# Kernel optimization log

Measured on AMD Instinct MI355X. Metric: run time of the kernel, lower is better.

## Reference

```python
import jax, jax.numpy as jnp
import numpy as np

H = 1024   # hidden_size
A = 16     # number_ab (branches)
O = 4      # num_outputs per branch
B = 4096   # batch
P = 2048   # number of selected rows
EPS = 1e-5


def setup_inputs() -> dict:
    key = jax.random.key(0)
    ks = jax.random.split(key, 12)
    s = 0.02  # weight init scale
    inp = {
        "X": jax.random.normal(ks[0], (B, H), jnp.float32),
        "X1": jax.random.normal(ks[1], (B, H), jnp.float32),
        # stacked per-branch parameters (batched over antibody axis A)
        "W1": jax.random.normal(ks[2], (A, H, H), jnp.float32) * s,
        "b1": jnp.zeros((A, H), jnp.float32),
        "W2": jax.random.normal(ks[3], (A, H, H), jnp.float32) * s,
        "b2": jnp.zeros((A, H), jnp.float32),
        "W3": jax.random.normal(ks[4], (A, H, H), jnp.float32) * s,
        "b3": jnp.zeros((A, H), jnp.float32),
        "gamma": jnp.ones((A, H), jnp.float32),
        "beta": jnp.zeros((A, H), jnp.float32),
        "W4": jax.random.normal(ks[5], (A, H, O), jnp.float32) * s,
        "b4": jnp.zeros((A, O), jnp.float32),
        "positions_y": jax.random.randint(ks[6], (P,), 0, B, jnp.int32),
    }
    return inp


def reference(X, X1, W1, b1, W2, b2, W3, b3, gamma, beta, W4, b4, positions_y):
    # z = l1(X) + l2(X1) per branch, batched over A: [B, A, H]
    z = (jnp.einsum('bh,aho->bao', X, W1) + b1
         + jnp.einsum('bh,aho->bao', X1, W2) + b2)
    # mlm: Linear -> ReLU -> LayerNorm -> Linear
    h = jax.nn.relu(jnp.einsum('bah,aho->bao', z, W3) + b3)  # [B, A, H]
    mu = jnp.mean(h, axis=-1, keepdims=True)
    var = jnp.var(h, axis=-1, keepdims=True)  # biased, matches nn.LayerNorm
    hn = (h - mu) / jnp.sqrt(var + EPS) * gamma + beta
    y = jnp.einsum('bah,aho->bao', hn, W4) + b4  # [B, A, O]
    # torch.cat along dim 1 over branches -> [B, A*O]
    Y = y.reshape(B, A * O)
    return Y[positions_y]
```

## Files before the change

### kernel.cpp

```cpp
#include <hip/hip_runtime.h>
#include <hip/hip_bf16.h>

using bf16 = __hip_bfloat16;
typedef __bf16 v8bf __attribute__((ext_vector_type(8)));
typedef float v4f __attribute__((ext_vector_type(4)));

#define H_ 1024
#define A_ 16
#define O_ 4
#define B_ 4096
#define P_ 2048
#define EPS_ 1e-5f

__device__ __forceinline__ void gl_lds16(const void* g, void* l) {
    __builtin_amdgcn_global_load_lds(
        (const __attribute__((address_space(1))) void*)g,
        (__attribute__((address_space(3))) void*)l, 16, 0, 0);
}

__global__ void addbias_k(const float* __restrict__ b1, const float* __restrict__ b2,
                          float* __restrict__ b12, int n) {
    int i = blockIdx.x * 256 + threadIdx.x;
    if (i < n) b12[i] = b1[i] + b2[i];
}

__global__ __launch_bounds__(256) void gather_k(const float* __restrict__ X,
                                                const float* __restrict__ X1,
                                                const int* __restrict__ pos,
                                                bf16* __restrict__ XX) {
    int p = blockIdx.x;
    int row = pos[p];
    const float4* x  = (const float4*)(X  + (size_t)row * H_);
    const float4* x1 = (const float4*)(X1 + (size_t)row * H_);
    bf16* o = XX + (size_t)p * (2 * H_);
    int i = threadIdx.x;
    float4 v = x[i];
    __align__(8) bf16 t[4];
    t[0] = __float2bfloat16(v.x); t[1] = __float2bfloat16(v.y);
    t[2] = __float2bfloat16(v.z); t[3] = __float2bfloat16(v.w);
    *(uint2*)(o + i * 4) = *(const uint2*)t;
    float4 w = x1[i];
    t[0] = __float2bfloat16(w.x); t[1] = __float2bfloat16(w.y);
    t[2] = __float2bfloat16(w.z); t[3] = __float2bfloat16(w.w);
    *(uint2*)(o + H_ + i * 4) = *(const uint2*)t;
}

__global__ __launch_bounds__(256) void transpose3_k(const float* __restrict__ W1s,
                                                    const float* __restrict__ W2s,
                                                    const float* __restrict__ W3s,
                                                    bf16* __restrict__ WT12,
                                                    bf16* __restrict__ WT3) {
    __shared__ float tile[64][65];
    const int which = blockIdx.z >> 4;
    const int a = blockIdx.z & 15;
    const float* src = (which == 0) ? W1s : (which == 1) ? W2s : W3s;
    bf16* dstBase = (which == 2) ? WT3 : WT12;
    const int dstK = (which == 2) ? H_ : 2 * H_;
    const int kOff = (which == 1) ? H_ : 0;

    const int k0 = blockIdx.x * 64;
    const int n0 = blockIdx.y * 64;
    const float* s = src + (size_t)a * H_ * H_;
    const int tc = threadIdx.x & 15;
    const int tr = threadIdx.x >> 4;
#pragma unroll
    for (int r = 0; r < 64; r += 16) {
        float4 v = *(const float4*)(s + (size_t)(k0 + tr + r) * H_ + n0 + tc * 4);
        tile[tr + r][tc * 4 + 0] = v.x;
        tile[tr + r][tc * 4 + 1] = v.y;
        tile[tr + r][tc * 4 + 2] = v.z;
        tile[tr + r][tc * 4 + 3] = v.w;
    }
    __syncthreads();
    bf16* d = dstBase + (size_t)a * H_ * dstK + kOff;
    const int wc = threadIdx.x & 7;
    const int wr = threadIdx.x >> 3;
#pragma unroll
    for (int r = 0; r < 64; r += 32) {
        const int n = wr + r;
        __align__(16) bf16 tmp[8];
#pragma unroll
        for (int j = 0; j < 8; j++) tmp[j] = __float2bfloat16(tile[wc * 8 + j][n]);
        *(uint4*)(d + (size_t)(n0 + n) * dstK + k0 + wc * 8) = *(const uint4*)tmp;
    }
}

template <bool RELU>
__global__ __launch_bounds__(256) void gemm_bt(const bf16* __restrict__ Amat, size_t aStrideA,
                                               const bf16* __restrict__ Bt,
                                               const float* __restrict__ bias,
                                               bf16* __restrict__ C,
                                               int M, int N, int K) {
    constexpr int BM = 128, BN = 128, BK = 32;
    __shared__ __align__(16) unsigned short As[BM * BK];
    __shared__ __align__(16) unsigned short Bs[BN * BK];

    const int a = blockIdx.z;
    const bf16* Ab = Amat + (size_t)a * aStrideA;
    const bf16* Bb = Bt + (size_t)a * (size_t)N * K;
    const int bm = blockIdx.x, bn = blockIdx.y;
    const int tid = threadIdx.x;
    const int lane = tid & 63;
    const int wave = tid >> 6;
    const int wm = (wave & 1) * 64;
    const int wn = (wave >> 1) * 64;

    v4f acc[4][4];
#pragma unroll
    for (int i = 0; i < 4; i++)
#pragma unroll
        for (int j = 0; j < 4; j++) acc[i][j] = (v4f){0.f, 0.f, 0.f, 0.f};

    const int r0 = tid >> 2;
    const int cs = (((tid & 3) ^ ((r0 >> 1) & 3))) * 8;
    const bf16* agBase = Ab + (size_t)(bm * BM + r0) * K + cs;
    const bf16* bgBase = Bb + (size_t)(bn * BN + r0) * K + cs;
    unsigned short* aLds0 = As + wave * 512;
    unsigned short* aLds1 = As + 2048 + wave * 512;
    unsigned short* bLds0 = Bs + wave * 512;
    unsigned short* bLds1 = Bs + 2048 + wave * 512;
    const size_t rowSkip = (size_t)64 * K;

    const int lr = lane & 15;
    const int q = lane >> 4;
    const int kq = (q ^ ((lr >> 1) & 3)) * 8;

    for (int k0 = 0; k0 < K; k0 += BK) {
        gl_lds16(agBase + k0, aLds0);
        gl_lds16(agBase + k0 + rowSkip, aLds1);
        gl_lds16(bgBase + k0, bLds0);
        gl_lds16(bgBase + k0 + rowSkip, bLds1);
        __syncthreads();
        v8bf af[4], bfr[4];
#pragma unroll
        for (int mi = 0; mi < 4; mi++)
            af[mi] = *(const v8bf*)(As + (wm + mi * 16 + lr) * BK + kq);
#pragma unroll
        for (int ni = 0; ni < 4; ni++)
            bfr[ni] = *(const v8bf*)(Bs + (wn + ni * 16 + lr) * BK + kq);
#pragma unroll
        for (int mi = 0; mi < 4; mi++)
#pragma unroll
            for (int ni = 0; ni < 4; ni++)
                acc[mi][ni] = __builtin_amdgcn_mfma_f32_16x16x32_bf16(af[mi], bfr[ni],
                                                                      acc[mi][ni], 0, 0, 0);
        __syncthreads();
    }

    const int lq = lane >> 4;
    bf16* Cb = C + (size_t)a * M * N;
#pragma unroll
    for (int ni = 0; ni < 4; ni++) {
        const int col = bn * BN + wn + ni * 16 + lr;
        const float bv = bias[(size_t)a * N + col];
#pragma unroll
        for (int mi = 0; mi < 4; mi++) {
            const int row0 = bm * BM + wm + mi * 16 + lq * 4;
#pragma unroll
            for (int rg = 0; rg < 4; rg++) {
                float v = acc[mi][ni][rg] + bv;
                if (RELU) v = v > 0.f ? v : 0.f;
                Cb[(size_t)(row0 + rg) * N + col] = __float2bfloat16(v);
            }
        }
    }
}

__global__ __launch_bounds__(256) void ln_head_k(const bf16* __restrict__ Hb,
                                                 const float* __restrict__ gamma,
                                                 const float* __restrict__ beta,
                                                 const float* __restrict__ W4,
                                                 const float* __restrict__ b4,
                                                 float* __restrict__ out) {
    int w = blockIdx.x * 4 + (threadIdx.x >> 6);
    int lane = threadIdx.x & 63;
    int a = w >> 11;
    int p = w & (P_ - 1);
    const bf16* hrow = Hb + ((size_t)a * P_ + p) * H_;
    float hv[16];
    float s = 0.f, ss = 0.f;
#pragma unroll
    for (int i = 0; i < 16; i++) {
        float v = __bfloat162float(hrow[lane + i * 64]);
        hv[i] = v;
        s += v;
        ss += v * v;
    }
#pragma unroll
    for (int off = 32; off; off >>= 1) {
        s += __shfl_xor(s, off);
        ss += __shfl_xor(ss, off);
    }
    float mu = s * (1.f / H_);
    float var = ss * (1.f / H_) - mu * mu;
    float rstd = rsqrtf(var + EPS_);
    const float* g = gamma + (size_t)a * H_;
    const float* be = beta + (size_t)a * H_;
    const float4* w4 = (const float4*)(W4 + (size_t)a * H_ * O_);
    float a0 = 0.f, a1 = 0.f, a2 = 0.f, a3 = 0.f;
#pragma unroll
    for (int i = 0; i < 16; i++) {
        int k = lane + i * 64;
        float hn = (hv[i] - mu) * rstd * g[k] + be[k];
        float4 wv = w4[k];
        a0 += hn * wv.x;
        a1 += hn * wv.y;
        a2 += hn * wv.z;
        a3 += hn * wv.w;
    }
#pragma unroll
    for (int off = 32; off; off >>= 1) {
        a0 += __shfl_xor(a0, off);
        a1 += __shfl_xor(a1, off);
        a2 += __shfl_xor(a2, off);
        a3 += __shfl_xor(a3, off);
    }
    if (lane < 4) {
        float v = (lane == 0 ? a0 : lane == 1 ? a1 : lane == 2 ? a2 : a3) + b4[a * O_ + lane];
        out[(size_t)p * (A_ * O_) + a * O_ + lane] = v;
    }
}

extern "C" void kernel_launch(void* const* d_in, const int* in_sizes, int n_in,
                              void* d_out, int out_size, void* d_ws, size_t ws_size,
                              hipStream_t stream) {
    const float* X     = (const float*)d_in[0];
    const float* X1    = (const float*)d_in[1];
    const float* W1    = (const float*)d_in[2];
    const float* b1    = (const float*)d_in[3];
    const float* W2    = (const float*)d_in[4];
    const float* b2    = (const float*)d_in[5];
    const float* W3    = (const float*)d_in[6];
    const float* b3    = (const float*)d_in[7];
    const float* gamma = (const float*)d_in[8];
    const float* beta  = (const float*)d_in[9];
    const float* W4    = (const float*)d_in[10];
    const float* b4    = (const float*)d_in[11];
    const int* pos     = (const int*)d_in[12];
    float* out = (float*)d_out;

    char* ws = (char*)d_ws;
    bf16* XX   = (bf16*)(ws);
    bf16* Z    = (bf16*)(ws + ((size_t)8 << 20));
    bf16* WT3  = (bf16*)(ws + ((size_t)72 << 20));
    bf16* WT12 = (bf16*)(ws + ((size_t)104 << 20));
    float* b12 = (float*)(ws + ((size_t)168 << 20));
    bf16* Hb   = WT12;

    addbias_k<<<(A_ * H_ + 255) / 256, 256, 0, stream>>>(b1, b2, b12, A_ * H_);
    gather_k<<<P_, 256, 0, stream>>>(X, X1, pos, XX);
    dim3 tgrid(H_ / 64, H_ / 64, 3 * A_);
    transpose3_k<<<tgrid, 256, 0, stream>>>(W1, W2, W3, WT12, WT3);

    dim3 g1(P_ / 128, H_ / 128, A_);
    gemm_bt<false><<<g1, 256, 0, stream>>>(XX, 0, WT12, b12, Z, P_, H_, 2 * H_);
    gemm_bt<true><<<g1, 256, 0, stream>>>(Z, (size_t)P_ * H_, WT3, b3, Hb, P_, H_, H_);

    ln_head_k<<<P_ * A_ / 4, 256, 0, stream>>>(Hb, gamma, beta, W4, b4, out);
}
```

Measured before the change: 549.9 us.

## Double-buffer LDS tiles in bf16 GEMM and remap blocks across XCDs

The GEMM mainloop now uses two LDS buffers per operand. The next K-tile's global-to-LDS loads are issued right after the barrier, so they overlap the MFMA work on the current tile, and one barrier per iteration is removed. Block indices are also recomputed from a linear block id, so blocks that share the same weight slice and branch land on the same XCD, which is meant to improve L2 reuse. The remap hardcodes a 16x8x16 grid, and the kernel now uses twice as much LDS, which may reduce occupancy.

```diff
diff --git a/kernel.cpp b/kernel.cpp
--- a/kernel.cpp
+++ b/kernel.cpp
@@ -92,13 +92,19 @@
                                                bf16* __restrict__ C,
                                                int M, int N, int K) {
     constexpr int BM = 128, BN = 128, BK = 32;
-    __shared__ __align__(16) unsigned short As[BM * BK];
-    __shared__ __align__(16) unsigned short Bs[BN * BK];
-
-    const int a = blockIdx.z;
+    __shared__ __align__(16) unsigned short As[2 * BM * BK];
+    __shared__ __align__(16) unsigned short Bs[2 * BN * BK];
+
+    const int L = blockIdx.x + 16 * blockIdx.y + 128 * blockIdx.z;
+    const int xcd = L & 7;
+    const int g = L >> 3;
+    const int bm = g & 15;
+    const int bna = xcd + 8 * (g >> 4);
+    const int bn = bna & 7;
+    const int a = bna >> 3;
+
     const bf16* Ab = Amat + (size_t)a * aStrideA;
     const bf16* Bb = Bt + (size_t)a * (size_t)N * K;
-    const int bm = blockIdx.x, bn = blockIdx.y;
     const int tid = threadIdx.x;
     const int lane = tid & 63;
     const int wave = tid >> 6;
@@ -115,36 +121,50 @@
     const int cs = (((tid & 3) ^ ((r0 >> 1) & 3))) * 8;
     const bf16* agBase = Ab + (size_t)(bm * BM + r0) * K + cs;
     const bf16* bgBase = Bb + (size_t)(bn * BN + r0) * K + cs;
-    unsigned short* aLds0 = As + wave * 512;
-    unsigned short* aLds1 = As + 2048 + wave * 512;
-    unsigned short* bLds0 = Bs + wave * 512;
-    unsigned short* bLds1 = Bs + 2048 + wave * 512;
     const size_t rowSkip = (size_t)64 * K;
+    const int w512 = wave * 512;
 
     const int lr = lane & 15;
     const int q = lane >> 4;
     const int kq = (q ^ ((lr >> 1) & 3)) * 8;
 
-    for (int k0 = 0; k0 < K; k0 += BK) {
-        gl_lds16(agBase + k0, aLds0);
-        gl_lds16(agBase + k0 + rowSkip, aLds1);
-        gl_lds16(bgBase + k0, bLds0);
-        gl_lds16(bgBase + k0 + rowSkip, bLds1);
+    const int nk = K / BK;
+
+    {
+        unsigned short* aB = As;
+        unsigned short* bB = Bs;
+        gl_lds16(agBase, aB + w512);
+        gl_lds16(agBase + rowSkip, aB + 2048 + w512);
+        gl_lds16(bgBase, bB + w512);
+        gl_lds16(bgBase + rowSkip, bB + 2048 + w512);
+    }
+
+    for (int kt = 0; kt < nk; ++kt) {
         __syncthreads();
+        if (kt + 1 < nk) {
+            const int k0 = (kt + 1) * BK;
+            unsigned short* aB = As + ((kt + 1) & 1) * 4096;
+            unsigned short* bB = Bs + ((kt + 1) & 1) * 4096;
+            gl_lds16(agBase + k0, aB + w512);
+            gl_lds16(agBase + k0 + rowSkip, aB + 2048 + w512);
+            gl_lds16(bgBase + k0, bB + w512);
+            gl_lds16(bgBase + k0 + rowSkip, bB + 2048 + w512);
+        }
+        const unsigned short* Ar = As + (kt & 1) * 4096;
+        const unsigned short* Br = Bs + (kt & 1) * 4096;
         v8bf af[4], bfr[4];
 #pragma unroll
         for (int mi = 0; mi < 4; mi++)
-            af[mi] = *(const v8bf*)(As + (wm + mi * 16 + lr) * BK + kq);
+            af[mi] = *(const v8bf*)(Ar + (wm + mi * 16 + lr) * BK + kq);
 #pragma unroll
         for (int ni = 0; ni < 4; ni++)
-            bfr[ni] = *(const v8bf*)(Bs + (wn + ni * 16 + lr) * BK + kq);
+            bfr[ni] = *(const v8bf*)(Br + (wn + ni * 16 + lr) * BK + kq);
 #pragma unroll
         for (int mi = 0; mi < 4; mi++)
 #pragma unroll
             for (int ni = 0; ni < 4; ni++)
                 acc[mi][ni] = __builtin_amdgcn_mfma_f32_16x16x32_bf16(af[mi], bfr[ni],
                                                                       acc[mi][ni], 0, 0, 0);
-        __syncthreads();
     }
 
     const int lq = lane >> 4;
```

Measured after the change: 527.3 us. 1.04x faster.
